# Optimization experiments

Measured on AMD Instinct MI355X. Metric: run time of the kernel, lower is better.

## Reference

```python
import jax, jax.numpy as jnp
import numpy as np

B, L, K, D = 1024, 128, 16, 512
NUM_FEATURES, NUM_LABELS, NUM_NEG = 100000, 131072, 2048
EPS = 0.1
C = 2.0 + EPS  # spherical kernel constant


def safe_log(x, eps=1e-08):
    return jnp.log(jnp.maximum(x, eps))


def safe_normalize(x, axis=-1, eps=0.0001):
    norm = jnp.linalg.norm(x, axis=axis, keepdims=True)
    return x / jnp.maximum(norm, eps)


def setup_inputs() -> dict:
    key = jax.random.key(0)
    k0, k1, k2, k3, k4 = jax.random.split(key, 5)
    indices = jax.random.randint(k0, (B, L), 0, NUM_FEATURES)
    mask = jnp.ones((B, L), jnp.float32)
    labels = jax.random.randint(k1, (B, K), 0, NUM_LABELS)
    label_mask = jnp.ones((B, K), jnp.float32)
    neg_indices = jax.random.randint(k2, (NUM_NEG,), 0, NUM_LABELS)
    embed_table = jax.random.normal(k3, (NUM_FEATURES, D), jnp.float32) * 0.02
    W_kernel = jax.random.normal(k4, (D, NUM_LABELS), jnp.float32) * 0.02  # nnx.Linear kernel (in, out)
    return {"indices": indices, "mask": mask, "labels": labels,
            "label_mask": label_mask, "neg_indices": neg_indices,
            "embed_table": embed_table, "W_kernel": W_kernel}


def reference(indices, mask, labels, label_mask, neg_indices, embed_table, W_kernel):
    # MeanEmbedding encoder
    embeds = embed_table[indices]                                  # [B, L, D]
    sum_embeds = jnp.sum(embeds * mask[:, :, None], axis=1)        # [B, D]
    enc = sum_embeds / jnp.maximum(jnp.sum(mask, axis=1, keepdims=True), 1.0)
    query = safe_normalize(enc, axis=-1)                           # [B, D]
    W = safe_normalize(W_kernel.T, axis=-1)                        # [NUM_LABELS, D]

    safe_labels = jnp.maximum(labels, 0)
    all_indices = jnp.concatenate([safe_labels.reshape(-1), neg_indices])  # [B*K + NN]
    W_subset = W[all_indices]                                      # [B*K+NN, D]

    # spherical Yat kernel: dot^2 / max(C - 2*dot, eps)
    dot = jnp.clip(query @ W_subset.T, -0.999, 0.999)              # [B, B*K+NN]
    scores = dot ** 2 / jnp.maximum(C - 2.0 * dot, EPS)

    idx_offsets = jnp.arange(B)[:, None] * K + jnp.arange(K)[None, :]
    pos_scores = jnp.take_along_axis(scores, idx_offsets, axis=1)  # [B, K]
    neg_scores = scores[:, B * K:]                                 # [B, NN]
    all_scores = jnp.concatenate([pos_scores, neg_scores], axis=1) + 1e-08
    log_Z = jax.scipy.special.logsumexp(safe_log(all_scores), axis=1)
    log_probs = safe_log(pos_scores + 1e-08) - log_Z[:, None]
    return -jnp.sum(log_probs * label_mask) / (jnp.sum(label_mask) + 1e-06)
```

## Files before the change

### kernel.cpp

```cpp
#include <hip/hip_runtime.h>
#include <hip/hip_bf16.h>

#define BDIM 1024
#define LDIM 128
#define KDIM 16
#define DDIM 512
#define NLAB 131072
#define NNEG 2048
#define NPOS (BDIM * KDIM)
#define NSUB (NPOS + NNEG)
#define EPSV 0.1f
#define CV 2.1f
#define NBUCK 512
#define QBLK (BDIM / 2)
#define GT_BLOCKS (NBUCK * 8)

typedef __attribute__((ext_vector_type(8))) short s8v;
typedef __attribute__((ext_vector_type(4))) float f4v;
typedef __attribute__((ext_vector_type(4))) float fv4;
typedef __attribute__((ext_vector_type(4))) unsigned short us4;

static __device__ __forceinline__ unsigned short f2bf(float x) {
    union { float f; unsigned u; } v; v.f = x;
    unsigned r = v.u + 0x7FFF + ((v.u >> 16) & 1);
    return (unsigned short)(r >> 16);
}
static __device__ __forceinline__ float bf2f(unsigned short h) {
    return __uint_as_float((unsigned)h << 16);
}

__global__ __launch_bounds__(256) void init_kernel(float* __restrict__ norms2,
                                                   float* __restrict__ Zrow,
                                                   float* __restrict__ accum,
                                                   int* __restrict__ ticket) {
    int j = blockIdx.x * 256 + threadIdx.x;
    if (j < NSUB) norms2[j] = 0.f;
    if (j < BDIM) Zrow[j] = 0.f;
    if (j < 2) accum[j] = 0.f;
    if (j == 0) *ticket = 0;
}

__global__ __launch_bounds__(1024) void sortall_kernel(const int* __restrict__ labels,
                                                       const int* __restrict__ negs,
                                                       int* __restrict__ offs_end,
                                                       int* __restrict__ cntg,
                                                       int* __restrict__ srt_v,
                                                       int* __restrict__ rank) {
    __shared__ int sc[NBUCK];
    int t = threadIdx.x;
    if (t < NBUCK) sc[t] = 0;
    __syncthreads();
    int vs[NSUB / 1024];
    #pragma unroll
    for (int k = 0; k < NSUB / 1024; ++k) {
        int j = k * 1024 + t;
        int v = (j < NPOS) ? max(labels[j], 0) : negs[j - NPOS];
        vs[k] = v;
        atomicAdd(&sc[v >> 8], 1);
    }
    __syncthreads();
    int c = (t < NBUCK) ? sc[t] : 0;
    for (int off = 1; off < NBUCK; off <<= 1) {
        int v2 = (t < NBUCK && t >= off) ? sc[t - off] : 0;
        __syncthreads();
        if (t < NBUCK) sc[t] += v2;
        __syncthreads();
    }
    if (t < NBUCK) { cntg[t] = c; sc[t] -= c; }
    __syncthreads();
    #pragma unroll
    for (int k = 0; k < NSUB / 1024; ++k) {
        int j = k * 1024 + t;
        int v = vs[k];
        int r = atomicAdd(&sc[v >> 8], 1);
        srt_v[r] = v;
        rank[j] = r;
    }
    __syncthreads();
    if (t < NBUCK) offs_end[t] = sc[t];
}

__global__ __launch_bounds__(256) void main1_kernel(const float* __restrict__ Wk,
                                                    const int* __restrict__ srt_v,
                                                    const int* __restrict__ offs_end,
                                                    const int* __restrict__ cnt,
                                                    unsigned short* __restrict__ WT,
                                                    float* __restrict__ norms2,
                                                    const int* __restrict__ indices,
                                                    const float* __restrict__ mask,
                                                    const float* __restrict__ embed,
                                                    float* __restrict__ query,
                                                    unsigned short* __restrict__ qbf) {
    __shared__ __align__(16) unsigned short tile[256][65];
    int t = threadIdx.x;
    int w = t >> 6, l = t & 63;

    if (blockIdx.x < QBLK) {
        int*   sidx  = (int*)&tile[0][0];
        float* smask = (float*)&tile[8][0];
        float* red   = (float*)&tile[17][0];
        float* snorm = (float*)&tile[18][0];
        int half = t >> 7;
        int tc = t & 127;
        int b = blockIdx.x * 2 + half;
        sidx[half * 128 + tc]  = indices[b * LDIM + tc];
        smask[half * 128 + tc] = mask[b * LDIM + tc];
        __syncthreads();
        float msum = 0.f;
        for (int i = 0; i < LDIM; ++i) msum += smask[half * 128 + i];
        fv4 acc = {0.f, 0.f, 0.f, 0.f};
        #pragma unroll 4
        for (int ll = 0; ll < LDIM; ++ll) {
            int   idx = sidx[half * 128 + ll];
            float m   = smask[half * 128 + ll];
            fv4 v = *(const fv4*)&embed[(size_t)idx * DDIM + tc * 4];
            acc += v * m;
        }
        float denom = fmaxf(msum, 1.0f);
        acc /= denom;
        float ss = acc[0] * acc[0] + acc[1] * acc[1] + acc[2] * acc[2] + acc[3] * acc[3];
        #pragma unroll
        for (int off = 32; off > 0; off >>= 1) ss += __shfl_xor(ss, off, 64);
        if (l == 0) red[w] = ss;
        __syncthreads();
        if (t == 0) {
            snorm[0] = sqrtf(red[0] + red[1]);
            snorm[1] = sqrtf(red[2] + red[3]);
        }
        __syncthreads();
        float inv = 1.f / fmaxf(snorm[half], 1e-4f);
        acc *= inv;
        __builtin_nontemporal_store(acc, (fv4*)&query[(size_t)b * DDIM + tc * 4]);
        us4 ob = { f2bf(acc[0]), f2bf(acc[1]), f2bf(acc[2]), f2bf(acc[3]) };
        __builtin_nontemporal_store(ob, (us4*)&qbf[(size_t)b * DDIM + tc * 4]);
    } else {
        int bt = blockIdx.x - QBLK;
        int g  = bt >> 3;
        int dt = bt & 7;
        int d0 = dt * 64;
        #pragma unroll
        for (int i = 0; i < 16; ++i) {
            int dl = w * 16 + i;
            fv4 v = __builtin_nontemporal_load(
                (const fv4*)&Wk[(size_t)(d0 + dl) * NLAB + g * 256 + l * 4]);
            tile[l * 4 + 0][dl] = f2bf(v[0]);
            tile[l * 4 + 1][dl] = f2bf(v[1]);
            tile[l * 4 + 2][dl] = f2bf(v[2]);
            tile[l * 4 + 3][dl] = f2bf(v[3]);
        }
        __syncthreads();
        int rend = offs_end[g];
        int rbeg = rend - cnt[g];
        for (int r = rbeg + w; r < rend; r += 4) {
            int v = srt_v[r];
            int col = v - g * 256;
            unsigned short h = tile[col][l];
            __builtin_nontemporal_store(h, &WT[(size_t)r * DDIM + d0 + l]);
            float f = bf2f(h);
            float ss = f * f;
            ss += __shfl_xor(ss, 1, 64);  ss += __shfl_xor(ss, 2, 64);
            ss += __shfl_xor(ss, 4, 64);  ss += __shfl_xor(ss, 8, 64);
            ss += __shfl_xor(ss, 16, 64); ss += __shfl_xor(ss, 32, 64);
            if (l == 0) atomicAdd(&norms2[r], ss);
        }
    }
}

static __device__ __forceinline__ float score_of(float acc, float nn) {
    float dot = acc / nn;
    dot = fminf(fmaxf(dot, -0.999f), 0.999f);
    return dot * dot / fmaxf(CV - 2.f * dot, EPSV);
}

__global__ __launch_bounds__(256) void main2_kernel(const unsigned short* __restrict__ qbf,
                                                    const float* __restrict__ query,
                                                    const unsigned short* __restrict__ WT,
                                                    const int* __restrict__ rank,
                                                    const float* __restrict__ norms2,
                                                    float* __restrict__ pos_scores,
                                                    float* __restrict__ Zrow) {
    int t = threadIdx.x;
    int w = t >> 6, l = t & 63;
    if (blockIdx.x < (BDIM / 64) * (NNEG / 64)) {
        __shared__ float rowsum[64];
        int bx = blockIdx.x;
        int mt = bx & 15, nt = bx >> 4;
        int wm = w >> 1, wn = w & 1;
        int lr = l & 15, lg = l >> 4;
        int m0 = mt * 64 + wm * 32;
        int n0 = nt * 64 + wn * 32;
        if (t < 64) rowsum[t] = 0.f;
        __syncthreads();

        int rB0 = rank[NPOS + n0 + lr];
        int rB1 = rank[NPOS + n0 + 16 + lr];
        const unsigned short* a0p = qbf + (size_t)(m0 + lr) * DDIM + lg * 8;
        const unsigned short* a1p = qbf + (size_t)(m0 + 16 + lr) * DDIM + lg * 8;
        const unsigned short* b0p = WT + (size_t)rB0 * DDIM + lg * 8;
        const unsigned short* b1p = WT + (size_t)rB1 * DDIM + lg * 8;

        f4v acc00 = {0.f, 0.f, 0.f, 0.f}, acc01 = acc00, acc10 = acc00, acc11 = acc00;
        #pragma unroll
        for (int k0 = 0; k0 < DDIM; k0 += 32) {
            s8v a0 = *(const s8v*)(a0p + k0);
            s8v a1 = *(const s8v*)(a1p + k0);
            s8v b0 = *(const s8v*)(b0p + k0);
            s8v b1 = *(const s8v*)(b1p + k0);
            acc00 = __builtin_amdgcn_mfma_f32_16x16x32_bf16(a0, b0, acc00, 0, 0, 0);
            acc01 = __builtin_amdgcn_mfma_f32_16x16x32_bf16(a0, b1, acc01, 0, 0, 0);
            acc10 = __builtin_amdgcn_mfma_f32_16x16x32_bf16(a1, b0, acc10, 0, 0, 0);
            acc11 = __builtin_amdgcn_mfma_f32_16x16x32_bf16(a1, b1, acc11, 0, 0, 0);
        }

        float nn0 = fmaxf(sqrtf(norms2[rB0]), 1e-4f);
        float nn1 = fmaxf(sqrtf(norms2[rB1]), 1e-4f);
        float s[8];
        #pragma unroll
        for (int i = 0; i < 4; ++i) {
            s[i]     = score_of(acc00[i], nn0) + score_of(acc01[i], nn1);
            s[4 + i] = score_of(acc10[i], nn0) + score_of(acc11[i], nn1);
        }
        #pragma unroll
        for (int i = 0; i < 8; ++i) {
            s[i] += __shfl_xor(s[i], 1, 64);
            s[i] += __shfl_xor(s[i], 2, 64);
            s[i] += __shfl_xor(s[i], 4, 64);
            s[i] += __shfl_xor(s[i], 8, 64);
        }
        if (lr == 0) {
            #pragma unroll
            for (int i = 0; i < 4; ++i) {
                atomicAdd(&rowsum[wm * 32 + lg * 4 + i], s[i]);
                atomicAdd(&rowsum[wm * 32 + 16 + lg * 4 + i], s[4 + i]);
            }
        }
        __syncthreads();
        if (t < 64) atomicAdd(&Zrow[mt * 64 + t], rowsum[t]);
    } else {
        int px = blockIdx.x - (BDIM / 64) * (NNEG / 64);
        int b = px * 4 + w;
        int j = b * KDIM + (l & 15);
        int r = rank[j];
        int g = l >> 4;
        const unsigned short* wrow = WT + (size_t)r * DDIM + g * 128;
        const float* qrow = query + (size_t)b * DDIM + g * 128;
        float acc = 0.f;
        #pragma unroll
        for (int kk = 0; kk < 128; kk += 8) {
            ushort4 w0 = *(const ushort4*)&wrow[kk];
            ushort4 w1 = *(const ushort4*)&wrow[kk + 4];
            float4 q0 = *(const float4*)&qrow[kk];
            float4 q1 = *(const float4*)&qrow[kk + 4];
            acc += bf2f(w0.x) * q0.x + bf2f(w0.y) * q0.y + bf2f(w0.z) * q0.z + bf2f(w0.w) * q0.w
                 + bf2f(w1.x) * q1.x + bf2f(w1.y) * q1.y + bf2f(w1.z) * q1.z + bf2f(w1.w) * q1.w;
        }
        acc += __shfl_xor(acc, 16, 64);
        acc += __shfl_xor(acc, 32, 64);
        if (l < 16) {
            float nrm = fmaxf(sqrtf(norms2[r]), 1e-4f);
            float dot = fminf(fmaxf(acc / nrm, -0.999f), 0.999f);
            float sc = dot * dot / fmaxf(CV - 2.f * dot, EPSV);
            pos_scores[j] = sc;
            float s = sc;
            s += __shfl_xor(s, 1, 64); s += __shfl_xor(s, 2, 64);
            s += __shfl_xor(s, 4, 64); s += __shfl_xor(s, 8, 64);
            if (l == 0) atomicAdd(&Zrow[b], s);
        }
    }
}

__global__ __launch_bounds__(256) void finalize_kernel(const float* __restrict__ pos_scores,
                                                       const float* __restrict__ label_mask,
                                                       const float* __restrict__ Zrow,
                                                       float* __restrict__ accum,
                                                       int* __restrict__ ticket,
                                                       float* __restrict__ out) {
    int j = blockIdx.x * 256 + threadIdx.x;
    int b = j >> 4;
    float lm = label_mask[j];
    float logZ = logf(Zrow[b] + (float)(KDIM + NNEG) * 1e-8f);
    float v = lm * (logf(pos_scores[j] + 1e-8f) - logZ);
    #pragma unroll
    for (int off = 32; off > 0; off >>= 1) {
        v  += __shfl_down(v, off, 64);
        lm += __shfl_down(lm, off, 64);
    }
    __shared__ float rv[4], rl[4];
    int wid = threadIdx.x >> 6, lane = threadIdx.x & 63;
    if (lane == 0) { rv[wid] = v; rl[wid] = lm; }
    __syncthreads();
    if (threadIdx.x == 0) {
        atomicAdd(&accum[0], rv[0] + rv[1] + rv[2] + rv[3]);
        atomicAdd(&accum[1], rl[0] + rl[1] + rl[2] + rl[3]);
        __threadfence();
        int old = atomicAdd(ticket, 1);
        if (old == (int)gridDim.x - 1) {
            float a = atomicAdd(&accum[0], 0.f);
            float m = atomicAdd(&accum[1], 0.f);
            out[0] = -a / (m + 1e-6f);
        }
    }
}

extern "C" void kernel_launch(void* const* d_in, const int* in_sizes, int n_in,
                              void* d_out, int out_size, void* d_ws, size_t ws_size,
                              hipStream_t stream) {
    const int*   indices    = (const int*)  d_in[0];
    const float* mask       = (const float*)d_in[1];
    const int*   labels     = (const int*)  d_in[2];
    const float* label_mask = (const float*)d_in[3];
    const int*   negs       = (const int*)  d_in[4];
    const float* embed      = (const float*)d_in[5];
    const float* Wk         = (const float*)d_in[6];
    float* out = (float*)d_out;

    unsigned short* WT  = (unsigned short*)d_ws;
    float* query      = (float*)(WT + (size_t)NSUB * DDIM);
    unsigned short* qbf = (unsigned short*)(query + (size_t)BDIM * DDIM);
    int*   srt_v      = (int*)(qbf + (size_t)BDIM * DDIM);
    int*   rank       = srt_v + NSUB;
    float* norms2     = (float*)(rank + NSUB);
    float* pos_scores = norms2 + NSUB;
    float* Zrow       = pos_scores + NPOS;
    float* accum      = Zrow + BDIM;
    int*   ticket     = (int*)(accum + 2);
    int*   cntg       = ticket + 1;
    int*   offs_end   = cntg + NBUCK;

    init_kernel<<<NSUB / 256, 256, 0, stream>>>(norms2, Zrow, accum, ticket);
    sortall_kernel<<<1, 1024, 0, stream>>>(labels, negs, offs_end, cntg, srt_v, rank);
    main1_kernel<<<QBLK + GT_BLOCKS, 256, 0, stream>>>(Wk, srt_v, offs_end, cntg, WT, norms2,
                                                       indices, mask, embed, query, qbf);
    main2_kernel<<<(BDIM / 64) * (NNEG / 64) + NPOS / 64, 256, 0, stream>>>(
        qbf, query, WT, rank, norms2, pos_scores, Zrow);
    finalize_kernel<<<NPOS / 256, 256, 0, stream>>>(pos_scores, label_mask, Zrow,
                                                    accum, ticket, out);
}
```

Baseline: 153.6 us.

## Split embedding-bag rows across four waves per query with LDS reduction

```diff
diff --git a/kernel.cpp b/kernel.cpp
--- a/kernel.cpp
+++ b/kernel.cpp
@@ -12,13 +12,11 @@
 #define EPSV 0.1f
 #define CV 2.1f
 #define NBUCK 512
-#define QBLK (BDIM / 2)
 #define GT_BLOCKS (NBUCK * 8)
 
 typedef __attribute__((ext_vector_type(8))) short s8v;
 typedef __attribute__((ext_vector_type(4))) float f4v;
 typedef __attribute__((ext_vector_type(4))) float fv4;
-typedef __attribute__((ext_vector_type(4))) unsigned short us4;
 
 static __device__ __forceinline__ unsigned short f2bf(float x) {
     union { float f; unsigned u; } v; v.f = x;
@@ -95,46 +93,57 @@
     int t = threadIdx.x;
     int w = t >> 6, l = t & 63;
 
-    if (blockIdx.x < QBLK) {
-        int*   sidx  = (int*)&tile[0][0];
-        float* smask = (float*)&tile[8][0];
-        float* red   = (float*)&tile[17][0];
-        float* snorm = (float*)&tile[18][0];
-        int half = t >> 7;
-        int tc = t & 127;
-        int b = blockIdx.x * 2 + half;
-        sidx[half * 128 + tc]  = indices[b * LDIM + tc];
-        smask[half * 128 + tc] = mask[b * LDIM + tc];
-        __syncthreads();
+    if (blockIdx.x < BDIM) {
+        char* base = (char*)&tile[0][0];
+        int*   sidx    = (int*)base;
+        float* smask   = (float*)(base + 512);
+        float* partial = (float*)(base + 1024);
+        float* red     = (float*)(base + 1024 + 8192);
+        float* snorm   = (float*)(base + 1024 + 8192 + 16);
+        int b = blockIdx.x;
+        if (t < LDIM) {
+            sidx[t]  = indices[b * LDIM + t];
+            smask[t] = mask[b * LDIM + t];
+        }
+        __syncthreads();
+        fv4 a0 = {0.f, 0.f, 0.f, 0.f}, a1 = {0.f, 0.f, 0.f, 0.f};
+        #pragma unroll 4
+        for (int i = 0; i < 32; ++i) {
+            int row = w * 32 + i;
+            int idx = sidx[row];
+            float m = smask[row];
+            const float* rp = &embed[(size_t)idx * DDIM + l * 8];
+            fv4 v0 = *(const fv4*)rp;
+            fv4 v1 = *(const fv4*)(rp + 4);
+            a0 += v0 * m;
+            a1 += v1 * m;
+        }
+        *(fv4*)&partial[w * 512 + l * 8]     = a0;
+        *(fv4*)&partial[w * 512 + l * 8 + 4] = a1;
         float msum = 0.f;
-        for (int i = 0; i < LDIM; ++i) msum += smask[half * 128 + i];
-        fv4 acc = {0.f, 0.f, 0.f, 0.f};
-        #pragma unroll 4
-        for (int ll = 0; ll < LDIM; ++ll) {
-            int   idx = sidx[half * 128 + ll];
-            float m   = smask[half * 128 + ll];
-            fv4 v = *(const fv4*)&embed[(size_t)idx * DDIM + tc * 4];
-            acc += v * m;
-        }
+        for (int i = 0; i < LDIM; ++i) msum += smask[i];
+        __syncthreads();
+        int c0 = t * 2;
+        float x = partial[c0]       + partial[512 + c0]     + partial[1024 + c0]     + partial[1536 + c0];
+        float y = partial[c0 + 1]   + partial[512 + c0 + 1] + partial[1024 + c0 + 1] + partial[1536 + c0 + 1];
         float denom = fmaxf(msum, 1.0f);
-        acc /= denom;
-        float ss = acc[0] * acc[0] + acc[1] * acc[1] + acc[2] * acc[2] + acc[3] * acc[3];
+        x /= denom; y /= denom;
+        float ss = x * x + y * y;
         #pragma unroll
         for (int off = 32; off > 0; off >>= 1) ss += __shfl_xor(ss, off, 64);
+        __syncthreads();
         if (l == 0) red[w] = ss;
         __syncthreads();
-        if (t == 0) {
-            snorm[0] = sqrtf(red[0] + red[1]);
-            snorm[1] = sqrtf(red[2] + red[3]);
-        }
-        __syncthreads();
-        float inv = 1.f / fmaxf(snorm[half], 1e-4f);
-        acc *= inv;
-        __builtin_nontemporal_store(acc, (fv4*)&query[(size_t)b * DDIM + tc * 4]);
-        us4 ob = { f2bf(acc[0]), f2bf(acc[1]), f2bf(acc[2]), f2bf(acc[3]) };
-        __builtin_nontemporal_store(ob, (us4*)&qbf[(size_t)b * DDIM + tc * 4]);
+        if (t == 0) snorm[0] = sqrtf(red[0] + red[1] + red[2] + red[3]);
+        __syncthreads();
+        float inv = 1.f / fmaxf(snorm[0], 1e-4f);
+        x *= inv; y *= inv;
+        float2 o = { x, y };
+        *(float2*)&query[(size_t)b * DDIM + c0] = o;
+        ushort2 ob = { f2bf(x), f2bf(y) };
+        *(ushort2*)&qbf[(size_t)b * DDIM + c0] = ob;
     } else {
-        int bt = blockIdx.x - QBLK;
+        int bt = blockIdx.x - BDIM;
         int g  = bt >> 3;
         int dt = bt & 7;
         int d0 = dt * 64;
@@ -329,7 +338,7 @@
 
     init_kernel<<<NSUB / 256, 256, 0, stream>>>(norms2, Zrow, accum, ticket);
     sortall_kernel<<<1, 1024, 0, stream>>>(labels, negs, offs_end, cntg, srt_v, rank);
-    main1_kernel<<<QBLK + GT_BLOCKS, 256, 0, stream>>>(Wk, srt_v, offs_end, cntg, WT, norms2,
+    main1_kernel<<<BDIM + GT_BLOCKS, 256, 0, stream>>>(Wk, srt_v, offs_end, cntg, WT, norms2,
                                                        indices, mask, embed, query, qbf);
     main2_kernel<<<(BDIM / 64) * (NNEG / 64) + NPOS / 64, 256, 0, stream>>>(
         qbf, query, WT, rank, norms2, pos_scores, Zrow);
```

New measurement: 152.0 us. About the same (-1.0%).
